# Performance work log

Hardware: AMD Instinct MI355X
Metric: run time of the kernel (lower is better)

The kernel has to match this reference:

```python
import jax, jax.numpy as jnp
import numpy as np


def _segmean(vals, idx, n):
    # PyG mean aggregation: sum over incoming edges / clamp(count, 1)
    s = jax.ops.segment_sum(vals, idx, num_segments=n)
    cnt = jax.ops.segment_sum(jnp.ones((idx.shape[0],), vals.dtype), idx, num_segments=n)
    return s / jnp.clip(cnt, 1.0)[:, None]


def setup_inputs() -> dict:
    key = jax.random.key(0)
    ks = jax.random.split(key, 18)
    NU, NI, D, H, O, E, L = 100000, 50000, 128, 256, 128, 800000, 400000
    sc = lambda d: 1.0 / np.sqrt(d)
    f32 = jnp.float32
    return {
        "x_user": jax.random.normal(ks[0], (NU, D), f32),
        "x_item": jax.random.normal(ks[1], (NI, D), f32),
        "edge_src": jax.random.randint(ks[2], (E,), 0, NU),
        "edge_dst": jax.random.randint(ks[3], (E,), 0, NI),
        "lbl_src": jax.random.randint(ks[4], (L,), 0, NU),
        "lbl_dst": jax.random.randint(ks[5], (L,), 0, NI),
        "wl1_ui": jax.random.normal(ks[6], (D, H), f32) * sc(D),
        "wr1_ui": jax.random.normal(ks[7], (D, H), f32) * sc(D),
        "b1_ui": jnp.zeros((H,), f32),
        "wl1_iu": jax.random.normal(ks[8], (D, H), f32) * sc(D),
        "wr1_iu": jax.random.normal(ks[9], (D, H), f32) * sc(D),
        "b1_iu": jnp.zeros((H,), f32),
        "wl2_ui": jax.random.normal(ks[10], (H, O), f32) * sc(H),
        "wr2_ui": jax.random.normal(ks[11], (H, O), f32) * sc(H),
        "b2_ui": jnp.zeros((O,), f32),
        "wl2_iu": jax.random.normal(ks[12], (H, O), f32) * sc(H),
        "wr2_iu": jax.random.normal(ks[13], (H, O), f32) * sc(H),
        "b2_iu": jnp.zeros((O,), f32),
    }


def reference(x_user, x_item, edge_src, edge_dst, lbl_src, lbl_dst,
              wl1_ui, wr1_ui, b1_ui, wl1_iu, wr1_iu, b1_iu,
              wl2_ui, wr2_ui, b2_ui, wl2_iu, wr2_iu, b2_iu):
    NU, NI = x_user.shape[0], x_item.shape[0]
    # Layer 1: hetero SAGEConv per edge type (user->item and item->user)
    agg_i = _segmean(x_user[edge_src], edge_dst, NI)  # [NI, D]
    agg_u = _segmean(x_item[edge_dst], edge_src, NU)  # [NU, D]
    h_item = jax.nn.relu(agg_i @ wl1_ui + x_item @ wr1_ui + b1_ui)  # [NI, H]
    h_user = jax.nn.relu(agg_u @ wl1_iu + x_user @ wr1_iu + b1_iu)  # [NU, H]
    # Layer 2
    agg_i2 = _segmean(h_user[edge_src], edge_dst, NI)  # [NI, H]
    agg_u2 = _segmean(h_item[edge_dst], edge_src, NU)  # [NU, H]
    z_item = agg_i2 @ wl2_ui + h_item @ wr2_ui + b2_ui  # [NI, O]
    z_user = agg_u2 @ wl2_iu + h_user @ wr2_iu + b2_iu  # [NU, O]
    # Decode: embedding gather + elementwise multiply + sum
    return (z_user[lbl_src] * z_item[lbl_dst]).sum(axis=-1)  # [L]
```

## Files before the change

### kernel.cpp

```cpp
#include <hip/hip_runtime.h>

#define DD 128
#define HH 256
#define OO 128

#define NBI 256
#define NBU 512

typedef unsigned short bf16_t;
typedef short bf16x8 __attribute__((ext_vector_type(8)));
typedef float f32x4 __attribute__((ext_vector_type(4)));

__device__ __forceinline__ float bf2f(bf16_t u) {
  union { unsigned int i; float f; } v; v.i = ((unsigned int)u) << 16; return v.f;
}
__device__ __forceinline__ bf16_t f2bf(float f) {
  union { float f; unsigned int i; } v; v.f = f;
  unsigned int r = v.i + 0x7FFFu + ((v.i >> 16) & 1u);
  return (bf16_t)(r >> 16);
}

__device__ __forceinline__ void acc8(float* acc, uint4 u) {
  const unsigned* p = (const unsigned*)&u;
#pragma unroll
  for (int i = 0; i < 4; ++i) {
    union { unsigned v; float f; } lo, hi;
    lo.v = p[i] << 16;
    hi.v = p[i] & 0xffff0000u;
    acc[2 * i] += lo.f;
    acc[2 * i + 1] += hi.f;
  }
}
__device__ __forceinline__ void unpack8(float* o, uint4 u) {
  const unsigned* p = (const unsigned*)&u;
#pragma unroll
  for (int i = 0; i < 4; ++i) {
    union { unsigned v; float f; } lo, hi;
    lo.v = p[i] << 16;
    hi.v = p[i] & 0xffff0000u;
    o[2 * i] = lo.f;
    o[2 * i + 1] = hi.f;
  }
}
__device__ __forceinline__ uint4 pack8(const float* v) {
  uint4 o; unsigned* p = (unsigned*)&o;
#pragma unroll
  for (int i = 0; i < 4; ++i)
    p[i] = (unsigned)f2bf(v[2 * i]) | ((unsigned)f2bf(v[2 * i + 1]) << 16);
  return o;
}

__global__ void probe_k(float* __restrict__ out, int n, float v) {
  int i = blockIdx.x * blockDim.x + threadIdx.x;
  if (i < n) out[i] = v;
}

__global__ __launch_bounds__(256) void hist_k(
    const int* __restrict__ src, const int* __restrict__ dst,
    int* __restrict__ hist_u, int* __restrict__ hist_i,
    int E, int Wi, int Wu) {
  __shared__ int hi[NBI], hu[NBU];
  int tid = threadIdx.x;
  for (int t = tid; t < NBI; t += 256) hi[t] = 0;
  for (int t = tid; t < NBU; t += 256) hu[t] = 0;
  __syncthreads();
  int base = blockIdx.x * 4096;
#pragma unroll
  for (int j = 0; j < 16; ++j) {
    int e = base + tid + j * 256;
    if (e < E) {
      atomicAdd(&hi[dst[e] / Wi], 1);
      atomicAdd(&hu[src[e] / Wu], 1);
    }
  }
  __syncthreads();
  for (int t = tid; t < NBI; t += 256) if (hi[t]) atomicAdd(hist_i + t, hi[t]);
  for (int t = tid; t < NBU; t += 256) if (hu[t]) atomicAdd(hist_u + t, hu[t]);
}

__global__ __launch_bounds__(512) void scan_small_pair_k(
    const int* __restrict__ hist_i, int* __restrict__ off_i, int* __restrict__ cur_i,
    const int* __restrict__ hist_u, int* __restrict__ off_u, int* __restrict__ cur_u) {
  __shared__ int lds[512];
  const int* hist = blockIdx.x ? hist_u : hist_i;
  int* off = blockIdx.x ? off_u : off_i;
  int* cur = blockIdx.x ? cur_u : cur_i;
  int n = blockIdx.x ? NBU : NBI;
  int t = threadIdx.x;
  int v = (t < n) ? hist[t] : 0;
  lds[t] = v; __syncthreads();
  for (int o = 1; o < 512; o <<= 1) {
    int tv = (t >= o) ? lds[t - o] : 0;
    __syncthreads(); lds[t] += tv; __syncthreads();
  }
  if (t < n) { int e = lds[t] - v; off[t] = e; cur[t] = e; }
}

__global__ __launch_bounds__(256) void bucket_append_k(
    const int* __restrict__ src, const int* __restrict__ dst, int E, int Wi, int Wu,
    int* __restrict__ cur_bi, int* __restrict__ cur_bu,
    unsigned int* __restrict__ ebuf_i, unsigned int* __restrict__ ebuf_u) {
  __shared__ int bi[NBI], bu[NBU];
  __shared__ uint2 es[4096];
  int tid = threadIdx.x;
  int base = blockIdx.x * 4096;
  int n = E - base; if (n > 4096) n = 4096;
  for (int t = tid; t < NBI; t += 256) bi[t] = 0;
  for (int t = tid; t < NBU; t += 256) bu[t] = 0;
  __syncthreads();
#pragma unroll
  for (int j = 0; j < 16; ++j) {
    int idx = tid + j * 256;
    if (idx < n) {
      int s = src[base + idx], d = dst[base + idx];
      es[idx] = make_uint2((unsigned)s, (unsigned)d);
      atomicAdd(&bi[d / Wi], 1);
      atomicAdd(&bu[s / Wu], 1);
    }
  }
  __syncthreads();
  for (int t = tid; t < NBI; t += 256) { int c = bi[t]; bi[t] = c ? atomicAdd(cur_bi + t, c) : 0; }
  for (int t = tid; t < NBU; t += 256) { int c = bu[t]; bu[t] = c ? atomicAdd(cur_bu + t, c) : 0; }
  __syncthreads();
#pragma unroll
  for (int j = 0; j < 16; ++j) {
    int idx = tid + j * 256;
    if (idx < n) {
      int s = (int)es[idx].x, d = (int)es[idx].y;
      int bI = d / Wi, bU = s / Wu;
      int pI = atomicAdd(&bi[bI], 1);
      int pU = atomicAdd(&bu[bU], 1);
      ebuf_i[pI] = ((unsigned)(d - bI * Wi) << 24) | (unsigned)s;
      ebuf_u[pU] = ((unsigned)(s - bU * Wu) << 24) | (unsigned)d;
    }
  }
}

__global__ __launch_bounds__(256) void bucket_fill2_k(
    const unsigned int* __restrict__ ebuf, const int* __restrict__ off,
    const int* __restrict__ endc, int* __restrict__ row,
    int* __restrict__ csr, int n, int W, int E) {
  int b = blockIdx.x;
  int d0 = b * W; if (d0 >= n) return;
  int cnt = n - d0; if (cnt > W) cnt = W;
  __shared__ int hist[320];
  __shared__ int cur[320];
  int tid = threadIdx.x;
  for (int t = tid; t < cnt; t += 256) hist[t] = 0;
  __syncthreads();
  int beg = off[b], e_end = endc[b];
  for (int e = beg + tid; e < e_end; e += 256)
    atomicAdd(&hist[ebuf[e] >> 24], 1);
  __syncthreads();
  if (tid < 64) {
    int lane = tid;
    int carry = beg;
    int nc = (cnt + 63) >> 6;
    for (int c = 0; c < nc; ++c) {
      int idx = (c << 6) + lane;
      int v = (idx < cnt) ? hist[idx] : 0;
      int x = v;
#pragma unroll
      for (int o = 1; o < 64; o <<= 1) { int t = __shfl_up(x, o); if (lane >= o) x += t; }
      if (idx < cnt) { int g = carry + x - v; row[d0 + idx] = g; cur[idx] = g; }
      carry += __shfl(x, 63);
    }
  }
  if (tid == 0 && d0 + cnt == n) row[n] = E;
  __syncthreads();
  for (int e = beg + tid; e < e_end; e += 256) {
    unsigned v = ebuf[e];
    int slot = atomicAdd(&cur[v >> 24], 1);
    csr[slot] = (int)(v & 0xFFFFFFu);
  }
}

__global__ void cvt_bf16_k(const float* __restrict__ in, bf16_t* __restrict__ out, int n4) {
  int i = blockIdx.x * blockDim.x + threadIdx.x;
  if (i < n4) {
    float4 v = ((const float4*)in)[i];
    ushort4 o; o.x = f2bf(v.x); o.y = f2bf(v.y); o.z = f2bf(v.z); o.w = f2bf(v.w);
    ((ushort4*)out)[i] = o;
  }
}

struct WBatch { const float* in[4]; bf16_t* out[4]; };
__global__ void twconv_batch_k(WBatch wb, int K, int N) {
  const float* __restrict__ in = wb.in[blockIdx.z];
  bf16_t* __restrict__ out = wb.out[blockIdx.z];
  __shared__ float t[32][33];
  int bx = blockIdx.x * 32, by = blockIdx.y * 32;
  int tx = threadIdx.x & 31, ty = threadIdx.x >> 5;
#pragma unroll
  for (int j = 0; j < 32; j += 8)
    t[ty + j][tx] = in[(size_t)(by + ty + j) * N + bx + tx];
  __syncthreads();
#pragma unroll
  for (int j = 0; j < 32; j += 8)
    out[(size_t)(bx + ty + j) * K + by + tx] = f2bf(t[tx][ty + j]);
}

struct GatherJob {
  const int* row; const int* csr;
  const bf16_t* X; bf16_t* agg; int n;
};

template<bool ADD>
__global__ void gather_mean16_k(GatherJob j0, GatherJob j1) {
  GatherJob j = blockIdx.y ? j1 : j0;
  int node = (int)(((long long)blockIdx.x * blockDim.x + threadIdx.x) >> 6);
  int lane = threadIdx.x & 63;
  if (node >= j.n) return;
  const int g = lane >> 4;
  const int l = lane & 15;
  int beg = j.row[node], end = j.row[node + 1];
  float acc[8] = {};
  for (int jj = beg; jj < end; jj += 64) {
    int cnt = min(64, end - jj);
    int my = (lane < cnt) ? j.csr[jj + lane] : 0;
    for (int k = 0; k < cnt; k += 4) {
      int idx = __shfl(my, k + g);
      if (k + g < cnt) {
        uint4 u = *(const uint4*)(j.X + (size_t)idx * 128 + l * 8);
        acc8(acc, u);
      }
    }
  }
#pragma unroll
  for (int m = 16; m < 64; m <<= 1)
#pragma unroll
    for (int i = 0; i < 8; ++i) acc[i] += __shfl_xor(acc[i], m);
  if (g == 0) {
    float inv = (end > beg) ? 1.0f / (float)(end - beg) : 0.0f;
    float v[8];
    if (ADD) {
      uint4 z = *(const uint4*)(j.agg + (size_t)node * 128 + l * 8);
      float zb[8]; unpack8(zb, z);
#pragma unroll
      for (int i = 0; i < 8; ++i) v[i] = acc[i] * inv + zb[i];
    } else {
#pragma unroll
      for (int i = 0; i < 8; ++i) v[i] = acc[i] * inv;
    }
    *(uint4*)(j.agg + (size_t)node * 128 + l * 8) = pack8(v);
  }
}

struct FJob {
  int M;
  const bf16_t* Aagg; const bf16_t* Axb;
  const bf16_t* W1; const bf16_t* W2;
  const float* b1;
  const bf16_t* Wc;
  const float* b2;
  bf16_t* Cz; bf16_t* Ct;
};

__global__ __launch_bounds__(256) void fused_gemm_k(FJob j0, FJob j1, int nbi) {
  const int bx = blockIdx.x;
  FJob j = (bx < nbi) ? j0 : j1;
  const int rb = (bx < nbi) ? bx : bx - nbi;
  const size_t row0 = (size_t)rb * 64;
  __shared__ __align__(16) bf16_t U[64 * 256];
  bf16_t* Aag = U;
  bf16_t* Axb = U + 64 * 128;
  bf16_t* Hls = U;
  char* Ub = (char*)U;
  const int tid = threadIdx.x;
  const int wave = tid >> 6, lane = tid & 63;
  const int wc = wave;
  const int l15 = lane & 15, l4 = lane >> 4;
  const int M = j.M;

#pragma unroll
  for (int jj = 0; jj < 4; ++jj) {
    int i = tid + jj * 256;
    int r = i >> 4, c = i & 15;
    size_t ar = row0 + r; if (ar >= (size_t)M) ar = M - 1;
    int cs = c ^ (r & 7);
    __builtin_amdgcn_global_load_lds(
        (const __attribute__((address_space(1))) void*)(j.Aagg + ar * 128 + cs * 8),
        (__attribute__((address_space(3))) void*)(Aag + i * 8), 16, 0, 0);
    __builtin_amdgcn_global_load_lds(
        (const __attribute__((address_space(1))) void*)(j.Axb + ar * 128 + cs * 8),
        (__attribute__((address_space(3))) void*)(Axb + i * 8), 16, 0, 0);
  }
  __syncthreads();

  f32x4 acc[4][4] = {};

#pragma unroll
  for (int kk = 0; kk < 4; ++kk) {
    bf16x8 aa[4], ax[4], bl[4], br[4];
#pragma unroll
    for (int mi = 0; mi < 4; ++mi) {
      int ra = mi * 16 + l15;
      int ch = (kk * 4 + l4) ^ (ra & 7);
      aa[mi] = *(const bf16x8*)(Aag + ra * 128 + ch * 8);
      ax[mi] = *(const bf16x8*)(Axb + ra * 128 + ch * 8);
    }
#pragma unroll
    for (int ni = 0; ni < 4; ++ni) {
      int c1 = wc * 64 + ni * 16 + l15;
      bl[ni] = *(const bf16x8*)(j.W1 + (size_t)c1 * 128 + kk * 32 + l4 * 8);
      br[ni] = *(const bf16x8*)(j.W2 + (size_t)c1 * 128 + kk * 32 + l4 * 8);
    }
#pragma unroll
    for (int mi = 0; mi < 4; ++mi)
#pragma unroll
      for (int ni = 0; ni < 4; ++ni)
        acc[mi][ni] = __builtin_amdgcn_mfma_f32_16x16x32_bf16(bl[ni], aa[mi], acc[mi][ni], 0, 0, 0);
#pragma unroll
    for (int mi = 0; mi < 4; ++mi)
#pragma unroll
      for (int ni = 0; ni < 4; ++ni)
        acc[mi][ni] = __builtin_amdgcn_mfma_f32_16x16x32_bf16(br[ni], ax[mi], acc[mi][ni], 0, 0, 0);
  }
  __syncthreads();

#pragma unroll
  for (int ni = 0; ni < 4; ++ni) {
    int c0 = wc * 64 + ni * 16 + l4 * 4;
    float4 bv = *(const float4*)(j.b1 + c0);
    const float* bp = (const float*)&bv;
#pragma unroll
    for (int mi = 0; mi < 4; ++mi) {
      int r = mi * 16 + l15;
      float v0 = fmaxf(acc[mi][ni][0] + bp[0], 0.f);
      float v1 = fmaxf(acc[mi][ni][1] + bp[1], 0.f);
      float v2 = fmaxf(acc[mi][ni][2] + bp[2], 0.f);
      float v3 = fmaxf(acc[mi][ni][3] + bp[3], 0.f);
      unsigned w0 = (unsigned)f2bf(v0) | ((unsigned)f2bf(v1) << 16);
      unsigned w1 = (unsigned)f2bf(v2) | ((unsigned)f2bf(v3) << 16);
      int p8 = (c0 >> 2) ^ ((r & 7) << 1);
      *(uint2*)(Ub + r * 512 + p8 * 8) = make_uint2(w0, w1);
    }
  }
  __syncthreads();

#pragma unroll
  for (int mi = 0; mi < 4; ++mi)
#pragma unroll
    for (int ni = 0; ni < 4; ++ni)
#pragma unroll
      for (int q = 0; q < 4; ++q) acc[mi][ni][q] = 0.f;

#pragma unroll
  for (int kk = 0; kk < 8; ++kk) {
    bf16x8 ah[4], bw[4];
#pragma unroll
    for (int mi = 0; mi < 4; ++mi) {
      int r2 = mi * 16 + l15;
      int ch = (kk * 4 + l4) ^ (r2 & 7);
      ah[mi] = *(const bf16x8*)(Hls + r2 * 256 + ch * 8);
    }
#pragma unroll
    for (int ni = 0; ni < 4; ++ni) {
      int c2 = wc * 64 + ni * 16 + l15;
      bw[ni] = *(const bf16x8*)(j.Wc + (size_t)c2 * 256 + kk * 32 + l4 * 8);
    }
#pragma unroll
    for (int mi = 0; mi < 4; ++mi)
#pragma unroll
      for (int ni = 0; ni < 4; ++ni)
        acc[mi][ni] = __builtin_amdgcn_mfma_f32_16x16x32_bf16(bw[ni], ah[mi], acc[mi][ni], 0, 0, 0);
  }
  __syncthreads();

#pragma unroll
  for (int ni = 0; ni < 4; ++ni) {
    int c0 = wc * 64 + ni * 16 + l4 * 4;
    float b0 = 0.f, b1v = 0.f, b2v = 0.f, b3v = 0.f;
    if (c0 < 128) {
      float4 bv = *(const float4*)(j.b2 + c0);
      b0 = bv.x; b1v = bv.y; b2v = bv.z; b3v = bv.w;
    }
#pragma unroll
    for (int mi = 0; mi < 4; ++mi) {
      int r = mi * 16 + l15;
      unsigned w0 = (unsigned)f2bf(acc[mi][ni][0] + b0) | ((unsigned)f2bf(acc[mi][ni][1] + b1v) << 16);
      unsigned w1 = (unsigned)f2bf(acc[mi][ni][2] + b2v) | ((unsigned)f2bf(acc[mi][ni][3] + b3v) << 16);
      int p8 = (c0 >> 2) ^ ((r & 7) << 1);
      *(uint2*)(Ub + r * 512 + p8 * 8) = make_uint2(w0, w1);
    }
  }
  __syncthreads();

#pragma unroll
  for (int p = 0; p < 8; ++p) {
    int s = tid + p * 256;
    int r = s >> 5, c16 = s & 31;
    size_t gr = row0 + r;
    if (gr < (size_t)M) {
      uint4 v = *(const uint4*)(Ub + r * 512 + (c16 ^ (r & 7)) * 16);
      if (c16 < 16) *(uint4*)(j.Cz + gr * 128 + c16 * 8) = v;
      else          *(uint4*)(j.Ct + gr * 128 + (c16 - 16) * 8) = v;
    }
  }
}

__global__ void decode16_k(const int* __restrict__ ls, const int* __restrict__ ld,
                           const bf16_t* __restrict__ zu, const bf16_t* __restrict__ zi,
                           float* __restrict__ out, int L) {
  long long gid = (long long)blockIdx.x * blockDim.x + threadIdx.x;
  int w = (int)(gid >> 4);
  int l = (int)(gid & 15);
  if (w >= L) return;
  int su = ls[w], si = ld[w];
  uint4 a = *(const uint4*)(zu + (size_t)su * OO + l * 8);
  uint4 b = *(const uint4*)(zi + (size_t)si * OO + l * 8);
  const unsigned* pa = (const unsigned*)&a;
  const unsigned* pb = (const unsigned*)&b;
  float sum = 0.f;
#pragma unroll
  for (int i = 0; i < 4; ++i) {
    union { unsigned v; float f; } la, ha, lb, hb;
    la.v = pa[i] << 16;        ha.v = pa[i] & 0xffff0000u;
    lb.v = pb[i] << 16;        hb.v = pb[i] & 0xffff0000u;
    sum += la.f * lb.f + ha.f * hb.f;
  }
#pragma unroll
  for (int m = 1; m < 16; m <<= 1) sum += __shfl_xor(sum, m);
  if (l == 0) out[w] = sum;
}

extern "C" void kernel_launch(void* const* d_in, const int* in_sizes, int n_in,
                              void* d_out, int out_size, void* d_ws, size_t ws_size,
                              hipStream_t stream) {
  const float* x_user = (const float*)d_in[0];
  const float* x_item = (const float*)d_in[1];
  const int* edge_src = (const int*)d_in[2];
  const int* edge_dst = (const int*)d_in[3];
  const int* lbl_src  = (const int*)d_in[4];
  const int* lbl_dst  = (const int*)d_in[5];
  const float* wl1_ui = (const float*)d_in[6];
  const float* wr1_ui = (const float*)d_in[7];
  const float* b1_ui  = (const float*)d_in[8];
  const float* wl1_iu = (const float*)d_in[9];
  const float* wr1_iu = (const float*)d_in[10];
  const float* b1_iu  = (const float*)d_in[11];
  const float* wl2_ui = (const float*)d_in[12];
  const float* wr2_ui = (const float*)d_in[13];
  const float* b2_ui  = (const float*)d_in[14];
  const float* wl2_iu = (const float*)d_in[15];
  const float* wr2_iu = (const float*)d_in[16];
  const float* b2_iu  = (const float*)d_in[17];

  const int NU = in_sizes[0] / DD;
  const int NI = in_sizes[1] / DD;
  const int E  = in_sizes[2];
  const int L  = in_sizes[4];
  const int Wi = (NI + NBI - 1) / NBI;
  const int Wu = (NU + NBU - 1) / NBU;
  const int nEB = (E + 4095) / 4096;

  size_t off = 0;
  auto take = [&](size_t bytes) { size_t o = off; off = (off + bytes + 255) & ~(size_t)255; return o; };
  char* base = (char*)d_ws;
  int* hist_i = (int*)(base + take(((size_t)NBI + NBU) * 4));
  int* hist_u = hist_i + NBI;
  size_t zeroB = ((size_t)NBI + NBU) * 4;
  int* row_i = (int*)(base + take((size_t)(NI + 1) * 4));
  int* row_u = (int*)(base + take((size_t)(NU + 1) * 4));
  int* off_i = (int*)(base + take((size_t)NBI * 4));
  int* off_u = (int*)(base + take((size_t)NBU * 4));
  int* cur_bi = (int*)(base + take((size_t)NBI * 4));
  int* cur_bu = (int*)(base + take((size_t)NBU * 4));
  int* csr_i = (int*)(base + take((size_t)E * 4));
  int* csr_u = (int*)(base + take((size_t)E * 4));
  unsigned int* ebuf_i = (unsigned int*)(base + take((size_t)E * 4));
  unsigned int* ebuf_u = (unsigned int*)(base + take((size_t)E * 4));
  bf16_t* pool = (bf16_t*)(base + take((size_t)(NI + NU) * HH * 2));
  bf16_t* agg_i   = pool;
  bf16_t* agg_u   = agg_i + (size_t)NI * DD;
  bf16_t* xb_item = agg_u + (size_t)NU * DD;
  bf16_t* xb_user = xb_item + (size_t)NI * DD;
  bf16_t* t_user = (bf16_t*)(base + take((size_t)(NI + NU) * OO * 2));
  bf16_t* t_item = t_user + (size_t)NU * OO;
  bf16_t* z_item = (bf16_t*)(base + take((size_t)(NI + NU) * OO * 2));
  bf16_t* z_user = z_item + (size_t)NI * OO;
  bf16_t* Wt1[4];
  for (int w = 0; w < 4; ++w) Wt1[w] = (bf16_t*)(base + take((size_t)HH * DD * 2));
  bf16_t* Wcat_item = (bf16_t*)(base + take((size_t)2 * OO * HH * 2));
  bf16_t* Wcat_user = (bf16_t*)(base + take((size_t)2 * OO * HH * 2));
  size_t need = off;

  float* out = (float*)d_out;
  if (ws_size < need || Wi > 320 || Wu > 320) {
    probe_k<<<(L + 255) / 256, 256, 0, stream>>>(out, L, (float)(ws_size >> 20));
    return;
  }

  hipMemsetAsync(hist_i, 0, zeroB, stream);
  hist_k<<<nEB, 256, 0, stream>>>(edge_src, edge_dst, hist_u, hist_i, E, Wi, Wu);
  scan_small_pair_k<<<2, 512, 0, stream>>>(hist_i, off_i, cur_bi, hist_u, off_u, cur_bu);
  bucket_append_k<<<nEB, 256, 0, stream>>>(edge_src, edge_dst, E, Wi, Wu, cur_bi, cur_bu, ebuf_i, ebuf_u);
  bucket_fill2_k<<<NBI, 256, 0, stream>>>(ebuf_i, off_i, cur_bi, row_i, csr_i, NI, Wi, E);
  bucket_fill2_k<<<NBU, 256, 0, stream>>>(ebuf_u, off_u, cur_bu, row_u, csr_u, NU, Wu, E);

  cvt_bf16_k<<<(NI * DD / 4 + 255) / 256, 256, 0, stream>>>(x_item, xb_item, NI * DD / 4);
  cvt_bf16_k<<<(NU * DD / 4 + 255) / 256, 256, 0, stream>>>(x_user, xb_user, NU * DD / 4);
  {
    WBatch w1;
    w1.in[0] = wl1_ui; w1.out[0] = Wt1[0];
    w1.in[1] = wr1_ui; w1.out[1] = Wt1[1];
    w1.in[2] = wl1_iu; w1.out[2] = Wt1[2];
    w1.in[3] = wr1_iu; w1.out[3] = Wt1[3];
    dim3 g1(HH / 32, DD / 32, 4);
    twconv_batch_k<<<g1, 256, 0, stream>>>(w1, DD, HH);
    WBatch w2;
    w2.in[0] = wr2_ui; w2.out[0] = Wcat_item;
    w2.in[1] = wl2_iu; w2.out[1] = Wcat_item + (size_t)OO * HH;
    w2.in[2] = wr2_iu; w2.out[2] = Wcat_user;
    w2.in[3] = wl2_ui; w2.out[3] = Wcat_user + (size_t)OO * HH;
    dim3 g2(OO / 32, HH / 32, 4);
    twconv_batch_k<<<g2, 256, 0, stream>>>(w2, HH, OO);
  }

  const int nbMax = ((NU > NI ? NU : NI) * 64 + 255) / 256;
  const int nbi64 = (NI + 63) / 64, nbu64 = (NU + 63) / 64;

  {
    GatherJob gi = { row_i, csr_i, xb_user, agg_i, NI };
    GatherJob gu = { row_u, csr_u, xb_item, agg_u, NU };
    gather_mean16_k<false><<<dim3(nbMax, 2), 256, 0, stream>>>(gi, gu);
  }

  {
    FJob ji = { NI, agg_i, xb_item, Wt1[0], Wt1[1], b1_ui, Wcat_item, b2_ui, z_item, t_item };
    FJob ju = { NU, agg_u, xb_user, Wt1[2], Wt1[3], b1_iu, Wcat_user, b2_iu, z_user, t_user };
    fused_gemm_k<<<nbi64 + nbu64, 256, 0, stream>>>(ji, ju, nbi64);
  }

  {
    GatherJob gi = { row_i, csr_i, t_user, z_item, NI };
    GatherJob gu = { row_u, csr_u, t_item, z_user, NU };
    gather_mean16_k<true><<<dim3(nbMax, 2), 256, 0, stream>>>(gi, gu);
  }

  decode16_k<<<(int)(((long long)L * 16 + 255) / 256), 256, 0, stream>>>(lbl_src, lbl_dst, z_user, z_item, out, L);
}
```

Before: 358.1 us.

## Make fused GEMM persistent with producer/consumer waves and double-buffered tiles

Replaces the one-tile-per-block fused two-layer GEMM with a persistent kernel of 256 blocks of 512 threads. Four waves compute layer-1 (agg and self GEMM plus ReLU) into a double-buffered LDS H tile while the other four waves compute layer-2 on the previous tile, and the next input tile is prefetched asynchronously. Weights and biases stay in registers across tiles, and outputs are written directly from registers. This aims to hide global load latency and weight reloads, at the cost of heavy register pressure, 128KB of LDS per block and a fixed grid split between the item and user jobs.

```diff
diff --git a/kernel.cpp b/kernel.cpp
--- a/kernel.cpp
+++ b/kernel.cpp
@@ -256,145 +256,163 @@
   bf16_t* Cz; bf16_t* Ct;
 };
 
-__global__ __launch_bounds__(256) void fused_gemm_k(FJob j0, FJob j1, int nbi) {
+__global__ __launch_bounds__(512, 2) void fused_pipe_k(FJob j0, FJob j1, int nbI, int nbU) {
   const int bx = blockIdx.x;
-  FJob j = (bx < nbi) ? j0 : j1;
-  const int rb = (bx < nbi) ? bx : bx - nbi;
-  const size_t row0 = (size_t)rb * 64;
-  __shared__ __align__(16) bf16_t U[64 * 256];
-  bf16_t* Aag = U;
-  bf16_t* Axb = U + 64 * 128;
-  bf16_t* Hls = U;
-  char* Ub = (char*)U;
+  const bool isU = bx >= nbI;
+  FJob j = isU ? j1 : j0;
+  const int lb = isU ? bx - nbI : bx;
+  const int NBLK = isU ? nbU : nbI;
+  const int M = j.M;
+  const int tiles = (M + 63) >> 6;
+  const int T = (tiles > lb) ? (tiles - lb + NBLK - 1) / NBLK : 0;
+
+  __shared__ __align__(16) bf16_t Ab[2][64 * 256];
+  __shared__ __align__(16) bf16_t Hb[2][64 * 256];
+
   const int tid = threadIdx.x;
   const int wave = tid >> 6, lane = tid & 63;
-  const int wc = wave;
+  const int wc = wave & 3;
   const int l15 = lane & 15, l4 = lane >> 4;
-  const int M = j.M;
-
-#pragma unroll
-  for (int jj = 0; jj < 4; ++jj) {
-    int i = tid + jj * 256;
-    int r = i >> 4, c = i & 15;
-    size_t ar = row0 + r; if (ar >= (size_t)M) ar = M - 1;
-    int cs = c ^ (r & 7);
-    __builtin_amdgcn_global_load_lds(
-        (const __attribute__((address_space(1))) void*)(j.Aagg + ar * 128 + cs * 8),
-        (__attribute__((address_space(3))) void*)(Aag + i * 8), 16, 0, 0);
-    __builtin_amdgcn_global_load_lds(
-        (const __attribute__((address_space(1))) void*)(j.Axb + ar * 128 + cs * 8),
-        (__attribute__((address_space(3))) void*)(Axb + i * 8), 16, 0, 0);
-  }
-  __syncthreads();
-
-  f32x4 acc[4][4] = {};
-
-#pragma unroll
-  for (int kk = 0; kk < 4; ++kk) {
-    bf16x8 aa[4], ax[4], bl[4], br[4];
-#pragma unroll
-    for (int mi = 0; mi < 4; ++mi) {
-      int ra = mi * 16 + l15;
-      int ch = (kk * 4 + l4) ^ (ra & 7);
-      aa[mi] = *(const bf16x8*)(Aag + ra * 128 + ch * 8);
-      ax[mi] = *(const bf16x8*)(Axb + ra * 128 + ch * 8);
-    }
+
+  auto STAGE = [&](int tt, int b) {
+    size_t row0 = (size_t)(lb + tt * NBLK) * 64;
+#pragma unroll
+    for (int jj = 0; jj < 2; ++jj) {
+      int i = tid + jj * 512;
+      int r = i >> 4, c = i & 15;
+      size_t ar = row0 + r; if (ar >= (size_t)M) ar = M - 1;
+      int cs = c ^ (r & 7);
+      __builtin_amdgcn_global_load_lds(
+          (const __attribute__((address_space(1))) void*)(j.Aagg + ar * 128 + cs * 8),
+          (__attribute__((address_space(3))) void*)(&Ab[b][0] + i * 8), 16, 0, 0);
+      __builtin_amdgcn_global_load_lds(
+          (const __attribute__((address_space(1))) void*)(j.Axb + ar * 128 + cs * 8),
+          (__attribute__((address_space(3))) void*)(&Ab[b][64 * 128] + i * 8), 16, 0, 0);
+    }
+  };
+
+  if (T > 0) STAGE(0, 0);
+  __syncthreads();
+
+  if (wave < 4) {
+    bf16x8 wA1[4][4], wA2[4][4];
+#pragma unroll
+    for (int kk = 0; kk < 4; ++kk)
+#pragma unroll
+      for (int ni = 0; ni < 4; ++ni) {
+        int c1 = wc * 64 + ni * 16 + l15;
+        wA1[kk][ni] = *(const bf16x8*)(j.W1 + (size_t)c1 * 128 + kk * 32 + l4 * 8);
+        wA2[kk][ni] = *(const bf16x8*)(j.W2 + (size_t)c1 * 128 + kk * 32 + l4 * 8);
+      }
+    float4 bias1[4];
+#pragma unroll
+    for (int ni = 0; ni < 4; ++ni)
+      bias1[ni] = *(const float4*)(j.b1 + wc * 64 + ni * 16 + l4 * 4);
+
+    for (int t = 0; t <= T; ++t) {
+      if (t + 1 < T) STAGE(t + 1, (t + 1) & 1);
+      if (t < T) {
+        const bf16_t* Aag = &Ab[t & 1][0];
+        const bf16_t* Axb = &Ab[t & 1][64 * 128];
+        char* Ub = (char*)&Hb[t & 1][0];
+        f32x4 acc[4][4] = {};
+#pragma unroll
+        for (int kk = 0; kk < 4; ++kk) {
+          bf16x8 aa[4], ax[4];
+#pragma unroll
+          for (int mi = 0; mi < 4; ++mi) {
+            int ra = mi * 16 + l15;
+            int ch = (kk * 4 + l4) ^ (ra & 7);
+            aa[mi] = *(const bf16x8*)(Aag + ra * 128 + ch * 8);
+            ax[mi] = *(const bf16x8*)(Axb + ra * 128 + ch * 8);
+          }
+#pragma unroll
+          for (int mi = 0; mi < 4; ++mi)
+#pragma unroll
+            for (int ni = 0; ni < 4; ++ni)
+              acc[mi][ni] = __builtin_amdgcn_mfma_f32_16x16x32_bf16(wA1[kk][ni], aa[mi], acc[mi][ni], 0, 0, 0);
+#pragma unroll
+          for (int mi = 0; mi < 4; ++mi)
+#pragma unroll
+            for (int ni = 0; ni < 4; ++ni)
+              acc[mi][ni] = __builtin_amdgcn_mfma_f32_16x16x32_bf16(wA2[kk][ni], ax[mi], acc[mi][ni], 0, 0, 0);
+        }
+#pragma unroll
+        for (int ni = 0; ni < 4; ++ni) {
+          int c0 = wc * 64 + ni * 16 + l4 * 4;
+          const float* bp = (const float*)&bias1[ni];
+#pragma unroll
+          for (int mi = 0; mi < 4; ++mi) {
+            int r = mi * 16 + l15;
+            float v0 = fmaxf(acc[mi][ni][0] + bp[0], 0.f);
+            float v1 = fmaxf(acc[mi][ni][1] + bp[1], 0.f);
+            float v2 = fmaxf(acc[mi][ni][2] + bp[2], 0.f);
+            float v3 = fmaxf(acc[mi][ni][3] + bp[3], 0.f);
+            unsigned w0 = (unsigned)f2bf(v0) | ((unsigned)f2bf(v1) << 16);
+            unsigned w1 = (unsigned)f2bf(v2) | ((unsigned)f2bf(v3) << 16);
+            int p8 = (c0 >> 2) ^ ((r & 7) << 1);
+            *(uint2*)(Ub + r * 512 + p8 * 8) = make_uint2(w0, w1);
+          }
+        }
+      }
+      __syncthreads();
+    }
+  } else {
+    bf16x8 wB[8][4];
+#pragma unroll
+    for (int kk = 0; kk < 8; ++kk)
+#pragma unroll
+      for (int ni = 0; ni < 4; ++ni) {
+        int c2 = wc * 64 + ni * 16 + l15;
+        wB[kk][ni] = *(const bf16x8*)(j.Wc + (size_t)c2 * 256 + kk * 32 + l4 * 8);
+      }
+    const bool isZ = (wc < 2);
+    float4 bias2[4];
 #pragma unroll
     for (int ni = 0; ni < 4; ++ni) {
-      int c1 = wc * 64 + ni * 16 + l15;
-      bl[ni] = *(const bf16x8*)(j.W1 + (size_t)c1 * 128 + kk * 32 + l4 * 8);
-      br[ni] = *(const bf16x8*)(j.W2 + (size_t)c1 * 128 + kk * 32 + l4 * 8);
-    }
-#pragma unroll
-    for (int mi = 0; mi < 4; ++mi)
-#pragma unroll
-      for (int ni = 0; ni < 4; ++ni)
-        acc[mi][ni] = __builtin_amdgcn_mfma_f32_16x16x32_bf16(bl[ni], aa[mi], acc[mi][ni], 0, 0, 0);
-#pragma unroll
-    for (int mi = 0; mi < 4; ++mi)
-#pragma unroll
-      for (int ni = 0; ni < 4; ++ni)
-        acc[mi][ni] = __builtin_amdgcn_mfma_f32_16x16x32_bf16(br[ni], ax[mi], acc[mi][ni], 0, 0, 0);
-  }
-  __syncthreads();
-
-#pragma unroll
-  for (int ni = 0; ni < 4; ++ni) {
-    int c0 = wc * 64 + ni * 16 + l4 * 4;
-    float4 bv = *(const float4*)(j.b1 + c0);
-    const float* bp = (const float*)&bv;
-#pragma unroll
-    for (int mi = 0; mi < 4; ++mi) {
-      int r = mi * 16 + l15;
-      float v0 = fmaxf(acc[mi][ni][0] + bp[0], 0.f);
-      float v1 = fmaxf(acc[mi][ni][1] + bp[1], 0.f);
-      float v2 = fmaxf(acc[mi][ni][2] + bp[2], 0.f);
-      float v3 = fmaxf(acc[mi][ni][3] + bp[3], 0.f);
-      unsigned w0 = (unsigned)f2bf(v0) | ((unsigned)f2bf(v1) << 16);
-      unsigned w1 = (unsigned)f2bf(v2) | ((unsigned)f2bf(v3) << 16);
-      int p8 = (c0 >> 2) ^ ((r & 7) << 1);
-      *(uint2*)(Ub + r * 512 + p8 * 8) = make_uint2(w0, w1);
-    }
-  }
-  __syncthreads();
-
-#pragma unroll
-  for (int mi = 0; mi < 4; ++mi)
-#pragma unroll
-    for (int ni = 0; ni < 4; ++ni)
-#pragma unroll
-      for (int q = 0; q < 4; ++q) acc[mi][ni][q] = 0.f;
-
-#pragma unroll
-  for (int kk = 0; kk < 8; ++kk) {
-    bf16x8 ah[4], bw[4];
-#pragma unroll
-    for (int mi = 0; mi < 4; ++mi) {
-      int r2 = mi * 16 + l15;
-      int ch = (kk * 4 + l4) ^ (r2 & 7);
-      ah[mi] = *(const bf16x8*)(Hls + r2 * 256 + ch * 8);
-    }
-#pragma unroll
-    for (int ni = 0; ni < 4; ++ni) {
-      int c2 = wc * 64 + ni * 16 + l15;
-      bw[ni] = *(const bf16x8*)(j.Wc + (size_t)c2 * 256 + kk * 32 + l4 * 8);
-    }
-#pragma unroll
-    for (int mi = 0; mi < 4; ++mi)
-#pragma unroll
-      for (int ni = 0; ni < 4; ++ni)
-        acc[mi][ni] = __builtin_amdgcn_mfma_f32_16x16x32_bf16(bw[ni], ah[mi], acc[mi][ni], 0, 0, 0);
-  }
-  __syncthreads();
-
-#pragma unroll
-  for (int ni = 0; ni < 4; ++ni) {
-    int c0 = wc * 64 + ni * 16 + l4 * 4;
-    float b0 = 0.f, b1v = 0.f, b2v = 0.f, b3v = 0.f;
-    if (c0 < 128) {
-      float4 bv = *(const float4*)(j.b2 + c0);
-      b0 = bv.x; b1v = bv.y; b2v = bv.z; b3v = bv.w;
-    }
-#pragma unroll
-    for (int mi = 0; mi < 4; ++mi) {
-      int r = mi * 16 + l15;
-      unsigned w0 = (unsigned)f2bf(acc[mi][ni][0] + b0) | ((unsigned)f2bf(acc[mi][ni][1] + b1v) << 16);
-      unsigned w1 = (unsigned)f2bf(acc[mi][ni][2] + b2v) | ((unsigned)f2bf(acc[mi][ni][3] + b3v) << 16);
-      int p8 = (c0 >> 2) ^ ((r & 7) << 1);
-      *(uint2*)(Ub + r * 512 + p8 * 8) = make_uint2(w0, w1);
-    }
-  }
-  __syncthreads();
-
-#pragma unroll
-  for (int p = 0; p < 8; ++p) {
-    int s = tid + p * 256;
-    int r = s >> 5, c16 = s & 31;
-    size_t gr = row0 + r;
-    if (gr < (size_t)M) {
-      uint4 v = *(const uint4*)(Ub + r * 512 + (c16 ^ (r & 7)) * 16);
-      if (c16 < 16) *(uint4*)(j.Cz + gr * 128 + c16 * 8) = v;
-      else          *(uint4*)(j.Ct + gr * 128 + (c16 - 16) * 8) = v;
+      int c0 = wc * 64 + ni * 16 + l4 * 4;
+      bias2[ni] = isZ ? *(const float4*)(j.b2 + c0) : make_float4(0.f, 0.f, 0.f, 0.f);
+    }
+    bf16_t* Co = isZ ? j.Cz : j.Ct;
+    const int ccbase = isZ ? wc * 64 : wc * 64 - 128;
+
+    for (int t = 0; t <= T; ++t) {
+      if (t + 1 < T) STAGE(t + 1, (t + 1) & 1);
+      if (t >= 1) {
+        const bf16_t* Hls = &Hb[(t - 1) & 1][0];
+        size_t row0 = (size_t)(lb + (t - 1) * NBLK) * 64;
+        f32x4 acc[4][4] = {};
+#pragma unroll
+        for (int kk = 0; kk < 8; ++kk) {
+          bf16x8 ah[4];
+#pragma unroll
+          for (int mi = 0; mi < 4; ++mi) {
+            int r2 = mi * 16 + l15;
+            int ch = (kk * 4 + l4) ^ (r2 & 7);
+            ah[mi] = *(const bf16x8*)(Hls + r2 * 256 + ch * 8);
+          }
+#pragma unroll
+          for (int mi = 0; mi < 4; ++mi)
+#pragma unroll
+            for (int ni = 0; ni < 4; ++ni)
+              acc[mi][ni] = __builtin_amdgcn_mfma_f32_16x16x32_bf16(wB[kk][ni], ah[mi], acc[mi][ni], 0, 0, 0);
+        }
+#pragma unroll
+        for (int ni = 0; ni < 4; ++ni) {
+          int cc = ccbase + ni * 16 + l4 * 4;
+          const float* bp = (const float*)&bias2[ni];
+#pragma unroll
+          for (int mi = 0; mi < 4; ++mi) {
+            size_t gr = row0 + mi * 16 + l15;
+            if (gr < (size_t)M) {
+              unsigned w0 = (unsigned)f2bf(acc[mi][ni][0] + bp[0]) | ((unsigned)f2bf(acc[mi][ni][1] + bp[1]) << 16);
+              unsigned w1 = (unsigned)f2bf(acc[mi][ni][2] + bp[2]) | ((unsigned)f2bf(acc[mi][ni][3] + bp[3]) << 16);
+              *(uint2*)(Co + gr * 128 + cc) = make_uint2(w0, w1);
+            }
+          }
+        }
+      }
+      __syncthreads();
     }
   }
 }
@@ -518,7 +536,7 @@
   }
 
   const int nbMax = ((NU > NI ? NU : NI) * 64 + 255) / 256;
-  const int nbi64 = (NI + 63) / 64, nbu64 = (NU + 63) / 64;
+  const int tiles_i = (NI + 63) / 64, tiles_u = (NU + 63) / 64;
 
   {
     GatherJob gi = { row_i, csr_i, xb_user, agg_i, NI };
@@ -527,9 +545,14 @@
   }
 
   {
+    int nbI = (int)((256LL * tiles_i) / (tiles_i + tiles_u));
+    if (nbI < 1) nbI = 1;
+    if (nbI > tiles_i) nbI = tiles_i;
+    int nbU2 = 256 - nbI;
+    if (nbU2 > tiles_u) nbU2 = tiles_u;
     FJob ji = { NI, agg_i, xb_item, Wt1[0], Wt1[1], b1_ui, Wcat_item, b2_ui, z_item, t_item };
     FJob ju = { NU, agg_u, xb_user, Wt1[2], Wt1[3], b1_iu, Wcat_user, b2_iu, z_user, t_user };
-    fused_gemm_k<<<nbi64 + nbu64, 256, 0, stream>>>(ji, ju, nbi64);
+    fused_pipe_k<<<nbI + nbU2, 512, 0, stream>>>(ji, ju, nbI, nbU2);
   }
 
   {
```

Measured after the change: 327.4 us. 8.6% less time.
